# Performance work log

Measured on AMD Instinct MI355X. Metric: run time of the kernel, lower is better.

The kernel has to match this reference:

```python
import jax, jax.numpy as jnp
import numpy as np

N_NODES = 50000
N_EDGES = 1_250_000
D_IN = 64
D_OUT = 64


def setup_inputs() -> dict:
    key = jax.random.key(0)
    k1, k2, k3, k4, k5 = jax.random.split(key, 5)
    feature = jax.random.normal(k1, (N_NODES, D_IN), dtype=jnp.float32)
    src = jax.random.randint(k2, (N_EDGES,), 0, N_NODES, dtype=jnp.int32)
    dst = jax.random.randint(k3, (N_EDGES,), 0, N_NODES, dtype=jnp.int32)
    W = jax.random.normal(k4, (D_OUT, D_IN), dtype=jnp.float32) * (1.0 / np.sqrt(D_IN))
    b = jax.random.normal(k5, (D_OUT,), dtype=jnp.float32) * 0.01
    return {"feature": feature, "src": src, "dst": dst, "W": W, "b": b}


def reference(feature, src, dst, W, b):
    # copy_u + sum: for each edge, message = feature[src]; reduce-sum at dst.
    msgs = feature[src]                                  # [E, D_IN] irregular gather
    h = jax.ops.segment_sum(msgs, dst, num_segments=N_NODES)  # [N, D_IN] scatter-add
    return h @ W.T + b                                   # nn.Linear
```

## Files before the change

kernel.cpp:

```cpp
#include <hip/hip_runtime.h>

#define D 64
#define SNB 256
#define CVB 128
#define NBP 1024
#define SCAP 5120
#define SLOTN 2048
#define NSTR 120
#define GPAD 16
#define SCAN_CHUNK 1024

static __device__ __forceinline__ unsigned short f2bf(float f) {
    unsigned u = __float_as_uint(f);
    unsigned r = (u + 0x7FFFu + ((u >> 16) & 1u)) >> 16;
    return (unsigned short)r;
}
static __device__ __forceinline__ float bf2f(unsigned short h) {
    return __uint_as_float((unsigned)h << 16);
}

__global__ void __launch_bounds__(1024)
build3_kernel(const int* __restrict__ src, const int* __restrict__ dst,
              int* __restrict__ gcur, unsigned* __restrict__ pairs,
              const float* __restrict__ feature, unsigned short* __restrict__ fbf,
              int n_edges, int nb, int chunk, int n4) {
    if (blockIdx.x >= SNB) {
        int i = (blockIdx.x - SNB) * 1024 + threadIdx.x;
        for (; i < n4; i += CVB * 1024) {
            float4 v = ((const float4*)feature)[i];
            ushort4 r;
            r.x = f2bf(v.x); r.y = f2bf(v.y); r.z = f2bf(v.z); r.w = f2bf(v.w);
            ((ushort4*)fbf)[i] = r;
        }
        return;
    }

    __shared__ unsigned inb[SCAP];
    __shared__ int hist[NBP];
    __shared__ int gpos[NBP];

    int blk = blockIdx.x, tid = threadIdx.x;

    for (int i = tid; i < NBP; i += 1024) hist[i] = 0;
    __syncthreads();

    int e0 = blk * chunk;
    int e1 = e0 + chunk; if (e1 > n_edges) e1 = n_edges;
    int m = e1 - e0;

    for (int i = tid; i < m; i += 1024) {
        int d_ = dst[e0 + i];
        int s_ = src[e0 + i];
        inb[i] = ((unsigned)(d_ >> 6) << 22) | ((unsigned)(d_ & 63) << 16) | (unsigned)s_;
        atomicAdd(&hist[d_ >> 6], 1);
    }
    __syncthreads();

    if (tid < nb) {
        int v = hist[tid];
        if (v > 0) {
            int gb = atomicAdd(&gcur[tid * GPAD], v);
            gpos[tid] = (gb + v <= SLOTN) ? (tid * SLOTN + gb) : (int)0x80000000;
        } else {
            gpos[tid] = (int)0x80000000;
        }
    }
    __syncthreads();

    for (int i = tid; i < m; i += 1024) {
        unsigned p = inb[i];
        int pos = atomicAdd(&gpos[p >> 22], 1);
        if (pos >= 0) pairs[pos] = p & 0x3FFFFFu;
    }
}

__global__ void __launch_bounds__(512, 8)
agg7_kernel(const unsigned short* __restrict__ fbf,
            const unsigned* __restrict__ pairs,
            const int* __restrict__ gcur,
            const float* __restrict__ W,
            const float* __restrict__ bias,
            float* __restrict__ out, int n_nodes) {
    __shared__ float4 WtSl[64 * 16];
    __shared__ float  H[64 * 65];
    __shared__ int cur[64];

    unsigned short* slist = (unsigned short*)WtSl;
    float4* Wt4 = WtSl;

    int tid = threadIdx.x;
    int lane = tid & 63, w = tid >> 6;
    int g = lane >> 4, sl = lane & 15;

    int bkt = blockIdx.x;
    int len = gcur[bkt * GPAD]; if (len > SLOTN) len = SLOTN;
    int e0 = bkt * SLOTN;

    if (tid < 64) cur[tid] = 0;
    __syncthreads();

    for (int i = tid; i < len; i += 512) {
        unsigned p = pairs[e0 + i];
        int ln = (p >> 16) & 63;
        int pos = atomicAdd(&cur[ln], 1);
        if (pos < NSTR) slist[ln * NSTR + pos] = (unsigned short)(p & 0xffffu);
    }
    __syncthreads();

#pragma unroll
    for (int qb = 0; qb < 2; ++qb) {
        int offq[4], dq[4];
        int dmax = 0;
#pragma unroll
        for (int qq = 0; qq < 4; ++qq) {
            int ln = w + (qb * 4 + qq) * 8;
            offq[qq] = ln * NSTR;
            int d = cur[ln]; if (d > NSTR) d = NSTR;
            dq[qq] = d;
            if (d > dmax) dmax = d;
        }
        float4 a4[4];
#pragma unroll
        for (int qq = 0; qq < 4; ++qq) { a4[qq].x = a4[qq].y = a4[qq].z = a4[qq].w = 0.f; }

        for (int j = 0; j < dmax; j += 8) {
            ushort4 u0[4], u1[4];
            float m0[4], m1[4];
#pragma unroll
            for (int qq = 0; qq < 4; ++qq) {
                int d = dq[qq];
                int i0 = j + g;
                int i1 = j + 4 + g;
                int ic0 = (i0 < d) ? i0 : ((d > 0) ? d - 1 : 0);
                int ic1 = (i1 < d) ? i1 : ((d > 0) ? d - 1 : 0);
                int s0 = slist[offq[qq] + ic0];
                int s1 = slist[offq[qq] + ic1];
                u0[qq] = *(const ushort4*)(fbf + s0 * D + sl * 4);
                u1[qq] = *(const ushort4*)(fbf + s1 * D + sl * 4);
                m0[qq] = (i0 < d) ? 1.f : 0.f;
                m1[qq] = (i1 < d) ? 1.f : 0.f;
            }
#pragma unroll
            for (int qq = 0; qq < 4; ++qq) {
                a4[qq].x += bf2f(u0[qq].x) * m0[qq];
                a4[qq].y += bf2f(u0[qq].y) * m0[qq];
                a4[qq].z += bf2f(u0[qq].z) * m0[qq];
                a4[qq].w += bf2f(u0[qq].w) * m0[qq];
                a4[qq].x += bf2f(u1[qq].x) * m1[qq];
                a4[qq].y += bf2f(u1[qq].y) * m1[qq];
                a4[qq].z += bf2f(u1[qq].z) * m1[qq];
                a4[qq].w += bf2f(u1[qq].w) * m1[qq];
            }
        }

#pragma unroll
        for (int qq = 0; qq < 4; ++qq) {
            float4 h = a4[qq];
            h.x += __shfl_xor(h.x, 16, 64);  h.y += __shfl_xor(h.y, 16, 64);
            h.z += __shfl_xor(h.z, 16, 64);  h.w += __shfl_xor(h.w, 16, 64);
            h.x += __shfl_xor(h.x, 32, 64);  h.y += __shfl_xor(h.y, 32, 64);
            h.z += __shfl_xor(h.z, 32, 64);  h.w += __shfl_xor(h.w, 32, 64);
            if (g == 0) {
                int ln = w + (qb * 4 + qq) * 8;
                H[ln * 65 + sl * 4 + 0] = h.x;
                H[ln * 65 + sl * 4 + 1] = h.y;
                H[ln * 65 + sl * 4 + 2] = h.z;
                H[ln * 65 + sl * 4 + 3] = h.w;
            }
        }
    }
    __syncthreads();

#pragma unroll
    for (int r = 0; r < 2; ++r) {
        int item = tid + r * 512;
        int k = item >> 4, oq = item & 15;
        float4 v;
        v.x = W[(4 * oq + 0) * 64 + k];
        v.y = W[(4 * oq + 1) * 64 + k];
        v.z = W[(4 * oq + 2) * 64 + k];
        v.w = W[(4 * oq + 3) * 64 + k];
        Wt4[k * 16 + oq] = v;
    }
    __syncthreads();

#pragma unroll
    for (int r = 0; r < 2; ++r) {
        int item = tid + r * 512;
        int ln = item >> 4, oq = item & 15;
        int n = bkt * 64 + ln;
        if (n < n_nodes) {
            float4 rv = *(const float4*)(bias + oq * 4);
#pragma unroll
            for (int k = 0; k < 64; ++k) {
                float hk = H[ln * 65 + k];
                float4 wv = Wt4[k * 16 + oq];
                rv.x += hk * wv.x; rv.y += hk * wv.y;
                rv.z += hk * wv.z; rv.w += hk * wv.w;
            }
            *(float4*)(out + n * D + oq * 4) = rv;
        }
    }
}


__global__ void hist_kernel(const int* __restrict__ dst, int* __restrict__ counts, int n_edges) {
    int e = blockIdx.x * blockDim.x + threadIdx.x;
    if (e < n_edges) atomicAdd(&counts[dst[e]], 1);
}

__global__ void reduce_kernel(const int* __restrict__ counts, int* __restrict__ partials, int n_nodes) {
    __shared__ int wsums[4];
    int tid = threadIdx.x;
    int base = blockIdx.x * SCAN_CHUNK + tid * 4;
    int s = 0;
#pragma unroll
    for (int i = 0; i < 4; ++i) {
        int idx = base + i;
        if (idx < n_nodes) s += counts[idx];
    }
    for (int o = 32; o > 0; o >>= 1) s += __shfl_down(s, o, 64);
    int lane = tid & 63, wave = tid >> 6;
    if (lane == 0) wsums[wave] = s;
    __syncthreads();
    if (tid == 0) partials[blockIdx.x] = wsums[0] + wsums[1] + wsums[2] + wsums[3];
}

__global__ void scan_partials_kernel(const int* __restrict__ partials, int* __restrict__ pscan, int nblk) {
    int lane = threadIdx.x;
    int v = (lane < nblk) ? partials[lane] : 0;
    int orig = v;
    for (int o = 1; o < 64; o <<= 1) {
        int y = __shfl_up(v, o, 64);
        if (lane >= o) v += y;
    }
    if (lane < nblk) pscan[lane] = v - orig;
}

__global__ void scan_kernel(const int* __restrict__ counts, const int* __restrict__ pscan,
                            int* __restrict__ offsets, int* __restrict__ cursors, int n_nodes) {
    __shared__ int wsums[4];
    int tid = threadIdx.x;
    int base = blockIdx.x * SCAN_CHUNK + tid * 4;
    int c[4];
    int tsum = 0;
#pragma unroll
    for (int i = 0; i < 4; ++i) {
        int idx = base + i;
        c[i] = (idx < n_nodes) ? counts[idx] : 0;
        tsum += c[i];
    }
    int lane = tid & 63, wave = tid >> 6;
    int x = tsum;
    for (int o = 1; o < 64; o <<= 1) {
        int y = __shfl_up(x, o, 64);
        if (lane >= o) x += y;
    }
    if (lane == 63) wsums[wave] = x;
    __syncthreads();
    int wpre = 0;
    for (int w = 0; w < wave; ++w) wpre += wsums[w];
    int excl = (x - tsum) + wpre + pscan[blockIdx.x];
#pragma unroll
    for (int i = 0; i < 4; ++i) {
        int idx = base + i;
        if (idx < n_nodes) { offsets[idx] = excl; cursors[idx] = excl; }
        excl += c[i];
    }
}

__global__ void fill_kernel(const int* __restrict__ src, const int* __restrict__ dst,
                            int* __restrict__ cursors, int* __restrict__ elist, int n_edges) {
    int e = blockIdx.x * blockDim.x + threadIdx.x;
    if (e < n_edges) {
        int pos = atomicAdd(&cursors[dst[e]], 1);
        elist[pos] = src[e];
    }
}

__global__ void agg_linear_kernel(const float* __restrict__ feature,
                                  const int* __restrict__ elist,
                                  const int* __restrict__ offsets,
                                  const int* __restrict__ counts,
                                  const float* __restrict__ W,
                                  const float* __restrict__ b,
                                  float* __restrict__ out,
                                  int n_nodes, int total_waves) {
    __shared__ float Wt[64 * 65];
    int tid = threadIdx.x;
    for (int i = tid; i < 64 * 64; i += 256) {
        int o = i >> 6, k = i & 63;
        Wt[k * 65 + o] = W[i];
    }
    __syncthreads();
    int lane = tid & 63;
    int waveId = (blockIdx.x * 256 + tid) >> 6;
    float bias = b[lane];
    for (int n = waveId; n < n_nodes; n += total_waves) {
        int off = offsets[n];
        int deg = counts[n];
        float acc = 0.f;
        int j = 0;
        for (; j + 4 <= deg; j += 4) {
            int s0 = elist[off + j + 0];
            int s1 = elist[off + j + 1];
            int s2 = elist[off + j + 2];
            int s3 = elist[off + j + 3];
            acc += feature[s0 * D + lane] + feature[s1 * D + lane]
                 + feature[s2 * D + lane] + feature[s3 * D + lane];
        }
        for (; j < deg; ++j) acc += feature[elist[off + j] * D + lane];
        float r = bias;
#pragma unroll
        for (int k = 0; k < 64; ++k) r += __shfl(acc, k, 64) * Wt[k * 65 + lane];
        out[n * D + lane] = r;
    }
}

__global__ void gcn_scatter_kernel(const float* __restrict__ feature,
                                   const int* __restrict__ src,
                                   const int* __restrict__ dst,
                                   float* __restrict__ out,
                                   int n_edges) {
    int e = blockIdx.x * 4 + (threadIdx.x >> 6);
    int lane = threadIdx.x & 63;
    if (e < n_edges) atomicAdd(&out[dst[e] * D + lane], feature[src[e] * D + lane]);
}

__global__ void gcn_linear_kernel(float* __restrict__ out,
                                  const float* __restrict__ W,
                                  const float* __restrict__ b,
                                  int n_nodes) {
    __shared__ float Wt[64 * 65];
    int tid = threadIdx.x;
    for (int i = tid; i < 64 * 64; i += 256) {
        int o = i >> 6, k = i & 63;
        Wt[k * 65 + o] = W[i];
    }
    __syncthreads();
    int lane = tid & 63;
    int n = blockIdx.x * 4 + (tid >> 6);
    if (n >= n_nodes) return;
    float val = out[n * D + lane];
    float acc = b[lane];
#pragma unroll
    for (int k = 0; k < 64; ++k) acc += __shfl(val, k, 64) * Wt[k * 65 + lane];
    out[n * D + lane] = acc;
}


extern "C" void kernel_launch(void* const* d_in, const int* in_sizes, int n_in,
                              void* d_out, int out_size, void* d_ws, size_t ws_size,
                              hipStream_t stream) {
    const float* feature = (const float*)d_in[0];
    const int* src       = (const int*)d_in[1];
    const int* dst       = (const int*)d_in[2];
    const float* W       = (const float*)d_in[3];
    const float* b       = (const float*)d_in[4];
    float* out           = (float*)d_out;

    int n_edges = in_sizes[1];
    int n_nodes = in_sizes[0] / D;

    int nb = (n_nodes + 63) >> 6;
    int chunk = (n_edges + SNB - 1) / SNB;
    int n4 = (n_nodes * D) / 4;

    size_t pairsWords = (size_t)nb * SLOTN;
    size_t needA = (size_t)NBP * GPAD * sizeof(int) + pairsWords * sizeof(int)
                 + (size_t)n_nodes * D * sizeof(unsigned short);

    if (n_nodes <= 65536 && nb <= NBP && chunk <= SCAP && ws_size >= needA) {
        int* gcur           = (int*)d_ws;
        unsigned* pairs     = (unsigned*)(gcur + (size_t)NBP * GPAD);
        unsigned short* fbf = (unsigned short*)(pairs + pairsWords);

        hipMemsetAsync(gcur, 0, (size_t)NBP * GPAD * sizeof(int), stream);
        build3_kernel<<<SNB + CVB, 1024, 0, stream>>>(src, dst, gcur, pairs,
                                                      feature, fbf,
                                                      n_edges, nb, chunk, n4);
        agg7_kernel<<<nb, 512, 0, stream>>>(fbf, pairs, gcur, W, b, out, n_nodes);
        return;
    }

    size_t needB = ((size_t)3 * n_nodes + 128 + (size_t)n_edges) * sizeof(int);
    int nblk_scan = (n_nodes + SCAN_CHUNK - 1) / SCAN_CHUNK;
    if (ws_size >= needB && nblk_scan <= 64) {
        int* counts   = (int*)d_ws;
        int* offsets  = counts + n_nodes;
        int* cursors  = offsets + n_nodes;
        int* partials = cursors + n_nodes;
        int* pscan    = partials + 64;
        int* elist    = pscan + 64;

        hipMemsetAsync(counts, 0, (size_t)n_nodes * sizeof(int), stream);
        hist_kernel<<<(n_edges + 255) / 256, 256, 0, stream>>>(dst, counts, n_edges);
        reduce_kernel<<<nblk_scan, 256, 0, stream>>>(counts, partials, n_nodes);
        scan_partials_kernel<<<1, 64, 0, stream>>>(partials, pscan, nblk_scan);
        scan_kernel<<<nblk_scan, 256, 0, stream>>>(counts, pscan, offsets, cursors, n_nodes);
        fill_kernel<<<(n_edges + 255) / 256, 256, 0, stream>>>(src, dst, cursors, elist, n_edges);
        agg_linear_kernel<<<3125, 256, 0, stream>>>(feature, elist, offsets, counts, W, b, out,
                                                    n_nodes, 3125 * 4);
        return;
    }

    hipMemsetAsync(d_out, 0, (size_t)out_size * sizeof(float), stream);
    gcn_scatter_kernel<<<(n_edges + 3) / 4, 256, 0, stream>>>(feature, src, dst, out, n_edges);
    gcn_linear_kernel<<<(n_nodes + 3) / 4, 256, 0, stream>>>(out, W, b, n_nodes);
}
```

Measured before the change: 136.3 us.

## Apply linear transform to node features before aggregation, gather pre-transformed rows

Uses linearity to compute feature @ W.T per node in the build kernel's converter blocks, storing the result as bf16. The aggregation kernel then only gathers and sums the transformed rows and adds bias, which removes the per-bucket W transpose and the 64x64 matmul stage. Shared-memory neighbour lists are pre-filled with a sentinel index pointing to an extra zero row, so padded lanes read zeros without per-element masking, and lanes now load 16-byte chunks. Rounding the transformed values to bf16 before summation changes numerical error, and the converter blocks now carry matmul work while running alongside the bucketing blocks.

```diff
diff --git a/kernel.cpp b/kernel.cpp
--- a/kernel.cpp
+++ b/kernel.cpp
@@ -2,7 +2,7 @@
 
 #define D 64
 #define SNB 256
-#define CVB 128
+#define CVB 192
 #define NBP 1024
 #define SCAP 5120
 #define SLOTN 2048
@@ -15,22 +15,56 @@
     unsigned r = (u + 0x7FFFu + ((u >> 16) & 1u)) >> 16;
     return (unsigned short)r;
 }
-static __device__ __forceinline__ float bf2f(unsigned short h) {
-    return __uint_as_float((unsigned)h << 16);
-}
 
 __global__ void __launch_bounds__(1024)
-build3_kernel(const int* __restrict__ src, const int* __restrict__ dst,
+build4_kernel(const int* __restrict__ src, const int* __restrict__ dst,
               int* __restrict__ gcur, unsigned* __restrict__ pairs,
-              const float* __restrict__ feature, unsigned short* __restrict__ fbf,
-              int n_edges, int nb, int chunk, int n4) {
+              const float* __restrict__ feature, const float* __restrict__ W,
+              unsigned short* __restrict__ fw,
+              int n_edges, int nb, int chunk, int n_nodes) {
     if (blockIdx.x >= SNB) {
-        int i = (blockIdx.x - SNB) * 1024 + threadIdx.x;
-        for (; i < n4; i += CVB * 1024) {
-            float4 v = ((const float4*)feature)[i];
-            ushort4 r;
-            r.x = f2bf(v.x); r.y = f2bf(v.y); r.z = f2bf(v.z); r.w = f2bf(v.w);
-            ((ushort4*)fbf)[i] = r;
+        __shared__ float4 Wt4c[64 * 16];
+        __shared__ float  Fs[64 * 68];
+        int tid = threadIdx.x;
+
+        if (blockIdx.x == SNB && tid < 16) {
+            ushort4 z; z.x = z.y = z.z = z.w = 0;
+            ((ushort4*)(fw + (size_t)n_nodes * D))[tid] = z;
+        }
+        {
+            int k = tid >> 4, oq = tid & 15;
+            float4 v;
+            v.x = W[(4 * oq + 0) * 64 + k];
+            v.y = W[(4 * oq + 1) * 64 + k];
+            v.z = W[(4 * oq + 2) * 64 + k];
+            v.w = W[(4 * oq + 3) * 64 + k];
+            Wt4c[k * 16 + oq] = v;
+        }
+        int r = tid >> 4, c4 = tid & 15;
+        for (int t = blockIdx.x - SNB; t < nb; t += CVB) {
+            int n = t * 64 + r;
+            int nc = (n < n_nodes) ? n : 0;
+            float4 fv = ((const float4*)(feature + (size_t)nc * 64))[c4];
+            __syncthreads();
+            Fs[r * 68 + c4 * 4 + 0] = fv.x;
+            Fs[r * 68 + c4 * 4 + 1] = fv.y;
+            Fs[r * 68 + c4 * 4 + 2] = fv.z;
+            Fs[r * 68 + c4 * 4 + 3] = fv.w;
+            __syncthreads();
+            float4 rv; rv.x = rv.y = rv.z = rv.w = 0.f;
+#pragma unroll
+            for (int k = 0; k < 64; ++k) {
+                float f = Fs[r * 68 + k];
+                float4 wv = Wt4c[k * 16 + c4];
+                rv.x += f * wv.x; rv.y += f * wv.y;
+                rv.z += f * wv.z; rv.w += f * wv.w;
+            }
+            if (n < n_nodes) {
+                ushort4 o;
+                o.x = f2bf(rv.x); o.y = f2bf(rv.y);
+                o.z = f2bf(rv.z); o.w = f2bf(rv.w);
+                ((ushort4*)(fw + (size_t)n * D))[c4] = o;
+            }
         }
         return;
     }
@@ -75,28 +109,26 @@
 }
 
 __global__ void __launch_bounds__(512, 8)
-agg7_kernel(const unsigned short* __restrict__ fbf,
+agg8_kernel(const unsigned short* __restrict__ fw,
             const unsigned* __restrict__ pairs,
             const int* __restrict__ gcur,
-            const float* __restrict__ W,
             const float* __restrict__ bias,
             float* __restrict__ out, int n_nodes) {
-    __shared__ float4 WtSl[64 * 16];
-    __shared__ float  H[64 * 65];
+    __shared__ unsigned short slist[64 * NSTR];
     __shared__ int cur[64];
 
-    unsigned short* slist = (unsigned short*)WtSl;
-    float4* Wt4 = WtSl;
-
     int tid = threadIdx.x;
-    int lane = tid & 63, w = tid >> 6;
-    int g = lane >> 4, sl = lane & 15;
-
     int bkt = blockIdx.x;
     int len = gcur[bkt * GPAD]; if (len > SLOTN) len = SLOTN;
     int e0 = bkt * SLOTN;
 
-    if (tid < 64) cur[tid] = 0;
+    {
+        unsigned short zs = (unsigned short)n_nodes;
+        unsigned zp = ((unsigned)zs << 16) | (unsigned)zs;
+        unsigned* s4 = (unsigned*)slist;
+        for (int i = tid; i < (64 * NSTR) / 2; i += 512) s4[i] = zp;
+        if (tid < 64) cur[tid] = 0;
+    }
     __syncthreads();
 
     for (int i = tid; i < len; i += 512) {
@@ -107,98 +139,68 @@
     }
     __syncthreads();
 
-#pragma unroll
-    for (int qb = 0; qb < 2; ++qb) {
-        int offq[4], dq[4];
-        int dmax = 0;
-#pragma unroll
-        for (int qq = 0; qq < 4; ++qq) {
-            int ln = w + (qb * 4 + qq) * 8;
-            offq[qq] = ln * NSTR;
-            int d = cur[ln]; if (d > NSTR) d = NSTR;
-            dq[qq] = d;
-            if (d > dmax) dmax = d;
-        }
-        float4 a4[4];
-#pragma unroll
-        for (int qq = 0; qq < 4; ++qq) { a4[qq].x = a4[qq].y = a4[qq].z = a4[qq].w = 0.f; }
-
-        for (int j = 0; j < dmax; j += 8) {
-            ushort4 u0[4], u1[4];
-            float m0[4], m1[4];
-#pragma unroll
-            for (int qq = 0; qq < 4; ++qq) {
-                int d = dq[qq];
-                int i0 = j + g;
-                int i1 = j + 4 + g;
-                int ic0 = (i0 < d) ? i0 : ((d > 0) ? d - 1 : 0);
-                int ic1 = (i1 < d) ? i1 : ((d > 0) ? d - 1 : 0);
-                int s0 = slist[offq[qq] + ic0];
-                int s1 = slist[offq[qq] + ic1];
-                u0[qq] = *(const ushort4*)(fbf + s0 * D + sl * 4);
-                u1[qq] = *(const ushort4*)(fbf + s1 * D + sl * 4);
-                m0[qq] = (i0 < d) ? 1.f : 0.f;
-                m1[qq] = (i1 < d) ? 1.f : 0.f;
+    int lane = tid & 63, w = tid >> 6;
+    int h  = lane >> 5;
+    int g  = (lane >> 3) & 3;
+    int sl = lane & 7;
+
+    float4 b0 = *(const float4*)(bias + sl * 8);
+    float4 b1 = *(const float4*)(bias + sl * 8 + 4);
+    const unsigned short* fwp = fw + sl * 8;
+
+    for (int qq = 0; qq < 4; ++qq) {
+        int ln = w * 8 + qq * 2 + h;
+        int d = cur[ln]; if (d > NSTR) d = NSTR;
+        { int dx = __shfl_xor(d, 32, 64); if (dx > d) d = dx; }
+        int off = ln * NSTR;
+
+        float4 aA, aB;
+        aA.x = aA.y = aA.z = aA.w = 0.f;
+        aB.x = aB.y = aB.z = aB.w = 0.f;
+
+        for (int j = 0; j < d; j += 8) {
+            int s0 = slist[off + j + g];
+            int s1 = slist[off + j + 4 + g];
+            uint4 v0 = *(const uint4*)(fwp + s0 * D);
+            uint4 v1 = *(const uint4*)(fwp + s1 * D);
+            aA.x += __uint_as_float(v0.x << 16);
+            aA.y += __uint_as_float(v0.x & 0xffff0000u);
+            aA.z += __uint_as_float(v0.y << 16);
+            aA.w += __uint_as_float(v0.y & 0xffff0000u);
+            aB.x += __uint_as_float(v0.z << 16);
+            aB.y += __uint_as_float(v0.z & 0xffff0000u);
+            aB.z += __uint_as_float(v0.w << 16);
+            aB.w += __uint_as_float(v0.w & 0xffff0000u);
+            aA.x += __uint_as_float(v1.x << 16);
+            aA.y += __uint_as_float(v1.x & 0xffff0000u);
+            aA.z += __uint_as_float(v1.y << 16);
+            aA.w += __uint_as_float(v1.y & 0xffff0000u);
+            aB.x += __uint_as_float(v1.z << 16);
+            aB.y += __uint_as_float(v1.z & 0xffff0000u);
+            aB.z += __uint_as_float(v1.w << 16);
+            aB.w += __uint_as_float(v1.w & 0xffff0000u);
+        }
+
+        aA.x += __shfl_xor(aA.x, 8, 64);  aA.y += __shfl_xor(aA.y, 8, 64);
+        aA.z += __shfl_xor(aA.z, 8, 64);  aA.w += __shfl_xor(aA.w, 8, 64);
+        aB.x += __shfl_xor(aB.x, 8, 64);  aB.y += __shfl_xor(aB.y, 8, 64);
+        aB.z += __shfl_xor(aB.z, 8, 64);  aB.w += __shfl_xor(aB.w, 8, 64);
+        aA.x += __shfl_xor(aA.x, 16, 64); aA.y += __shfl_xor(aA.y, 16, 64);
+        aA.z += __shfl_xor(aA.z, 16, 64); aA.w += __shfl_xor(aA.w, 16, 64);
+        aB.x += __shfl_xor(aB.x, 16, 64); aB.y += __shfl_xor(aB.y, 16, 64);
+        aB.z += __shfl_xor(aB.z, 16, 64); aB.w += __shfl_xor(aB.w, 16, 64);
+
+        if (g == 0) {
+            int n = bkt * 64 + ln;
+            if (n < n_nodes) {
+                float4 r0, r1;
+                r0.x = aA.x + b0.x; r0.y = aA.y + b0.y;
+                r0.z = aA.z + b0.z; r0.w = aA.w + b0.w;
+                r1.x = aB.x + b1.x; r1.y = aB.y + b1.y;
+                r1.z = aB.z + b1.z; r1.w = aB.w + b1.w;
+                *(float4*)(out + n * D + sl * 8)     = r0;
+                *(float4*)(out + n * D + sl * 8 + 4) = r1;
             }
-#pragma unroll
-            for (int qq = 0; qq < 4; ++qq) {
-                a4[qq].x += bf2f(u0[qq].x) * m0[qq];
-                a4[qq].y += bf2f(u0[qq].y) * m0[qq];
-                a4[qq].z += bf2f(u0[qq].z) * m0[qq];
-                a4[qq].w += bf2f(u0[qq].w) * m0[qq];
-                a4[qq].x += bf2f(u1[qq].x) * m1[qq];
-                a4[qq].y += bf2f(u1[qq].y) * m1[qq];
-                a4[qq].z += bf2f(u1[qq].z) * m1[qq];
-                a4[qq].w += bf2f(u1[qq].w) * m1[qq];
-            }
-        }
-
-#pragma unroll
-        for (int qq = 0; qq < 4; ++qq) {
-            float4 h = a4[qq];
-            h.x += __shfl_xor(h.x, 16, 64);  h.y += __shfl_xor(h.y, 16, 64);
-            h.z += __shfl_xor(h.z, 16, 64);  h.w += __shfl_xor(h.w, 16, 64);
-            h.x += __shfl_xor(h.x, 32, 64);  h.y += __shfl_xor(h.y, 32, 64);
-            h.z += __shfl_xor(h.z, 32, 64);  h.w += __shfl_xor(h.w, 32, 64);
-            if (g == 0) {
-                int ln = w + (qb * 4 + qq) * 8;
-                H[ln * 65 + sl * 4 + 0] = h.x;
-                H[ln * 65 + sl * 4 + 1] = h.y;
-                H[ln * 65 + sl * 4 + 2] = h.z;
-                H[ln * 65 + sl * 4 + 3] = h.w;
-            }
-        }
-    }
-    __syncthreads();
-
-#pragma unroll
-    for (int r = 0; r < 2; ++r) {
-        int item = tid + r * 512;
-        int k = item >> 4, oq = item & 15;
-        float4 v;
-        v.x = W[(4 * oq + 0) * 64 + k];
-        v.y = W[(4 * oq + 1) * 64 + k];
-        v.z = W[(4 * oq + 2) * 64 + k];
-        v.w = W[(4 * oq + 3) * 64 + k];
-        Wt4[k * 16 + oq] = v;
-    }
-    __syncthreads();
-
-#pragma unroll
-    for (int r = 0; r < 2; ++r) {
-        int item = tid + r * 512;
-        int ln = item >> 4, oq = item & 15;
-        int n = bkt * 64 + ln;
-        if (n < n_nodes) {
-            float4 rv = *(const float4*)(bias + oq * 4);
-#pragma unroll
-            for (int k = 0; k < 64; ++k) {
-                float hk = H[ln * 65 + k];
-                float4 wv = Wt4[k * 16 + oq];
-                rv.x += hk * wv.x; rv.y += hk * wv.y;
-                rv.z += hk * wv.z; rv.w += hk * wv.w;
-            }
-            *(float4*)(out + n * D + oq * 4) = rv;
         }
     }
 }
@@ -364,22 +366,21 @@
 
     int nb = (n_nodes + 63) >> 6;
     int chunk = (n_edges + SNB - 1) / SNB;
-    int n4 = (n_nodes * D) / 4;
 
     size_t pairsWords = (size_t)nb * SLOTN;
     size_t needA = (size_t)NBP * GPAD * sizeof(int) + pairsWords * sizeof(int)
-                 + (size_t)n_nodes * D * sizeof(unsigned short);
-
-    if (n_nodes <= 65536 && nb <= NBP && chunk <= SCAP && ws_size >= needA) {
-        int* gcur           = (int*)d_ws;
-        unsigned* pairs     = (unsigned*)(gcur + (size_t)NBP * GPAD);
-        unsigned short* fbf = (unsigned short*)(pairs + pairsWords);
+                 + (size_t)(n_nodes + 1) * D * sizeof(unsigned short);
+
+    if (n_nodes <= 65535 && nb <= NBP && chunk <= SCAP && ws_size >= needA) {
+        int* gcur          = (int*)d_ws;
+        unsigned* pairs    = (unsigned*)(gcur + (size_t)NBP * GPAD);
+        unsigned short* fw = (unsigned short*)(pairs + pairsWords);
 
         hipMemsetAsync(gcur, 0, (size_t)NBP * GPAD * sizeof(int), stream);
-        build3_kernel<<<SNB + CVB, 1024, 0, stream>>>(src, dst, gcur, pairs,
-                                                      feature, fbf,
-                                                      n_edges, nb, chunk, n4);
-        agg7_kernel<<<nb, 512, 0, stream>>>(fbf, pairs, gcur, W, b, out, n_nodes);
+        build4_kernel<<<SNB + CVB, 1024, 0, stream>>>(src, dst, gcur, pairs,
+                                                      feature, W, fw,
+                                                      n_edges, nb, chunk, n_nodes);
+        agg8_kernel<<<nb, 512, 0, stream>>>(fw, pairs, gcur, b, out, n_nodes);
         return;
     }
 
```

Result: faster. 128.2 us (-6.0%).
